# Kernel tuning notes

Measured on AMD Instinct MI355X. Metric: run time of the kernel, lower is better.

## Reference

```python
import math
import jax, jax.numpy as jnp
import numpy as np

B, N, D = 16, 2048, 64

def setup_inputs() -> dict:
    key = jax.random.key(0)
    kq, kk, kv, kl = jax.random.split(key, 4)
    q = jax.random.normal(kq, (B, N, D), dtype=jnp.float32)
    k = jax.random.normal(kk, (B, N, D), dtype=jnp.float32)
    v = jax.random.normal(kv, (B, N, D), dtype=jnp.float32)
    valid = jax.random.randint(kl, (B, N), 0, 2048, dtype=jnp.int64 if jax.config.jax_enable_x64 else jnp.int32)
    return {"q": q, "k": k, "v": v, "valid": valid}

def reference(q, k, v, valid):
    # scores[b,i,j] = <q[b,i], k[b,j]> / sqrt(d)
    d = k.shape[-1]
    scores = jnp.einsum('bid,bjd->bij', q, k) / jnp.sqrt(jnp.asarray(d, q.dtype))
    # mask[b,i,j] = (j+1) > valid[b,i]; masked positions replaced by 1e-6
    # (faithful to torch.masked_fill(scores, mask, 1e-06) -- NOT -inf)
    key_pos = jnp.arange(1, scores.shape[-1] + 1)  # [N]
    mask = key_pos[None, None, :] > valid[:, :, None]  # [B,N,N]
    mask_scores = jnp.where(mask, jnp.asarray(1e-06, scores.dtype), scores)
    weights = jax.nn.softmax(mask_scores, axis=-1)
    # dropout p=0.0 -> identity
    return jnp.einsum('bij,bjd->bid', weights, v)
```

## Files before the change

kernel.cpp:

```cpp
#include <hip/hip_runtime.h>
#include <hip/hip_bf16.h>
#include <stdint.h>

#define BB 16
#define NN 2048
#define DD 64
#define BM 64
#define BN 64
#define KSTR 72
#define PSTR 72

typedef __attribute__((ext_vector_type(8))) short short8;
typedef __attribute__((ext_vector_type(4))) float f32x4;

__device__ __forceinline__ unsigned short f2bf(float f) {
  union { float f; uint32_t u; } c; c.f = f;
  uint32_t u = c.u + 0x7fffu + ((c.u >> 16) & 1u);
  return (unsigned short)(u >> 16);
}
__device__ __forceinline__ uint32_t pkrn(float a, float b) {
  union { __hip_bfloat162 h; uint32_t u; } c;
  c.h = __float22bfloat162_rn(make_float2(a, b));
  return c.u;
}

__global__ __launch_bounds__(256) void prep_kernel(const float* __restrict__ k,
                                                   const float* __restrict__ v,
                                                   unsigned short* __restrict__ kbf,
                                                   unsigned short* __restrict__ vt) {
  __shared__ float t[64][65];
  int id = blockIdx.x, tid = threadIdx.x;
  if (id < 2048) {
    int i = id * 256 + tid;
    float4 f = ((const float4*)k)[i];
    ushort4 o;
    o.x = f2bf(f.x); o.y = f2bf(f.y); o.z = f2bf(f.z); o.w = f2bf(f.w);
    ((ushort4*)kbf)[i] = o;
  } else {
    int bid = id - 2048;
    int b = bid >> 5;
    int k0 = (bid & 31) * 64;
    const float4* src = (const float4*)(v + ((size_t)b * NN + k0) * DD);
#pragma unroll
    for (int i = 0; i < 4; i++) {
      int f4 = tid + i * 256;
      int row = f4 >> 4, c4 = f4 & 15;
      float4 f = src[f4];
      t[row][c4*4+0] = f.x; t[row][c4*4+1] = f.y; t[row][c4*4+2] = f.z; t[row][c4*4+3] = f.w;
    }
    __syncthreads();
    int d = tid >> 2, kg = tid & 3;
    unsigned short* dst = vt + ((size_t)b * DD + d) * NN + k0 + kg * 16;
#pragma unroll
    for (int u = 0; u < 4; u++) {
      ushort4 o;
      o.x = f2bf(t[kg*16+u*4+0][d]);
      o.y = f2bf(t[kg*16+u*4+1][d]);
      o.z = f2bf(t[kg*16+u*4+2][d]);
      o.w = f2bf(t[kg*16+u*4+3][d]);
      ((ushort4*)dst)[u] = o;
    }
  }
}

template <int NS>
__global__ __launch_bounds__(256, 4) void attn_kernel(
    const float* __restrict__ q, const unsigned short* __restrict__ kbf,
    const unsigned short* __restrict__ vtbf, const int* __restrict__ valid,
    float* __restrict__ out, unsigned short* __restrict__ po,
    float* __restrict__ pz)
{
  constexpr int JLEN = NN / NS;
  constexpr int ITERS = JLEN / BN;

  __shared__ __align__(16) unsigned short Klds[BN * KSTR];
  __shared__ __align__(16) unsigned short Vlds[DD * KSTR];
  __shared__ __align__(16) unsigned short Plds[4 * 16 * PSTR];
  __shared__ int vld[BM];

  int id = blockIdx.x;
  int b = (id & 7) + 8 * ((id >> 3) & 1);
  int rest = id >> 4;
  int sp = rest % NS;
  int qt = rest / NS;
  int i0 = qt * BM;
  int jbase = sp * JLEN;

  int tid = threadIdx.x;
  int w = tid >> 6;
  int lane = tid & 63;
  int m = lane & 15;
  int quad = lane >> 4;

  if (tid < BM) vld[tid] = valid[b * NN + i0 + tid];

  short8 qf[2];
  {
    const float* qp = q + ((size_t)b * NN + (i0 + w * 16 + m)) * DD;
#pragma unroll
    for (int s = 0; s < 2; s++) {
      float4 f0 = *(const float4*)(qp + s * 32 + quad * 8);
      float4 f1 = *(const float4*)(qp + s * 32 + quad * 8 + 4);
      union { short8 v; uint32_t x[4]; } tmp;
      tmp.x[0] = pkrn(f0.x * 0.125f, f0.y * 0.125f);
      tmp.x[1] = pkrn(f0.z * 0.125f, f0.w * 0.125f);
      tmp.x[2] = pkrn(f1.x * 0.125f, f1.y * 0.125f);
      tmp.x[3] = pkrn(f1.z * 0.125f, f1.w * 0.125f);
      qf[s] = tmp.v;
    }
  }

  __syncthreads();
  int vq = vld[w * 16 + m];

  f32x4 o[4] = {{0,0,0,0},{0,0,0,0},{0,0,0,0},{0,0,0,0}};
  float z = 0.0f;
  unsigned short* pbase = Plds + w * 16 * PSTR;

  int srow = tid >> 2, scol = (tid & 3) * 16;
  const unsigned short* gk = kbf + ((size_t)(b * NN + jbase + srow)) * DD + scol;
  const unsigned short* gv = vtbf + ((size_t)b * DD + srow) * NN + jbase + scol;

  uint4 ka = *(const uint4*)gk, kb2 = *(const uint4*)(gk + 8);
  uint4 va = *(const uint4*)gv, vb2 = *(const uint4*)(gv + 8);

  for (int it = 0; it < ITERS; ++it) {
    int j0 = jbase + it * BN;
    __syncthreads();
    *(uint4*)&Klds[srow * KSTR + scol]     = ka;
    *(uint4*)&Klds[srow * KSTR + scol + 8] = kb2;
    *(uint4*)&Vlds[srow * KSTR + scol]     = va;
    *(uint4*)&Vlds[srow * KSTR + scol + 8] = vb2;
    if (it + 1 < ITERS) {
      gk += BN * DD; gv += BN;
      ka = *(const uint4*)gk; kb2 = *(const uint4*)(gk + 8);
      va = *(const uint4*)gv; vb2 = *(const uint4*)(gv + 8);
    }
    __syncthreads();

    f32x4 s[4] = {{0,0,0,0},{0,0,0,0},{0,0,0,0},{0,0,0,0}};
#pragma unroll
    for (int c = 0; c < 4; c++) {
#pragma unroll
      for (int ss = 0; ss < 2; ss++) {
        short8 kf = *(const short8*)&Klds[(c * 16 + m) * KSTR + ss * 32 + quad * 8];
        s[c] = __builtin_amdgcn_mfma_f32_16x16x32_bf16(kf, qf[ss], s[c], 0, 0, 0);
      }
    }

#pragma unroll
    for (int c = 0; c < 4; c++) {
      float e[4];
#pragma unroll
      for (int rr = 0; rr < 4; rr++) {
        int j = j0 + c * 16 + quad * 4 + rr;
        float arg = (j < vq) ? s[c][rr] : 1.0e-6f;
        e[rr] = __expf(arg);
      }
      z += (e[0] + e[1]) + (e[2] + e[3]);
      *(uint2*)&pbase[m * PSTR + c * 16 + quad * 4] =
          make_uint2(pkrn(e[0], e[1]), pkrn(e[2], e[3]));
    }

    __builtin_amdgcn_s_waitcnt(0xc07f);

#pragma unroll
    for (int ss = 0; ss < 2; ss++) {
      short8 pf = *(const short8*)&pbase[m * PSTR + ss * 32 + quad * 8];
#pragma unroll
      for (int t = 0; t < 4; t++) {
        short8 vf = *(const short8*)&Vlds[(t * 16 + m) * KSTR + ss * 32 + quad * 8];
        o[t] = __builtin_amdgcn_mfma_f32_16x16x32_bf16(vf, pf, o[t], 0, 0, 0);
      }
    }
  }

  z += __shfl_xor(z, 16);
  z += __shfl_xor(z, 32);

  if (NS > 1) {
    int row = i0 + w * 16 + m;
    unsigned short* op = po + ((size_t)((sp * BB + b) * NN) + row) * DD;
#pragma unroll
    for (int t = 0; t < 4; t++)
      *(uint2*)&op[t * 16 + quad * 4] = make_uint2(pkrn(o[t][0], o[t][1]),
                                                   pkrn(o[t][2], o[t][3]));
    if (quad == 0) pz[(size_t)(sp * BB + b) * NN + row] = z;
  } else {
    float inv = 1.0f / z;
    int row = i0 + w * 16 + m;
    float* op = out + ((size_t)b * NN + row) * DD;
#pragma unroll
    for (int t = 0; t < 4; t++)
      *(float4*)&op[t * 16 + quad * 4] =
          make_float4(o[t][0]*inv, o[t][1]*inv, o[t][2]*inv, o[t][3]*inv);
  }
}

template <int NS>
__global__ __launch_bounds__(256) void combine_kernel(const unsigned short* __restrict__ po,
                                                      const float* __restrict__ pz,
                                                      float* __restrict__ out) {
  int gid = blockIdx.x * 256 + threadIdx.x;
  size_t base = (size_t)gid * 8;
  int rowz = gid >> 3;
  float r[8] = {0,0,0,0,0,0,0,0};
  float zs = 0.0f;
#pragma unroll
  for (int sp = 0; sp < NS; sp++) {
    uint4 a = *(const uint4*)(po + (size_t)sp * BB * NN * DD + base);
    zs += pz[(size_t)sp * BB * NN + rowz];
    uint32_t aw[4] = {a.x, a.y, a.z, a.w};
#pragma unroll
    for (int i = 0; i < 4; i++) {
      r[2*i]   += __uint_as_float(aw[i] << 16);
      r[2*i+1] += __uint_as_float(aw[i] & 0xffff0000u);
    }
  }
  float inv = 1.0f / zs;
  float4* op = (float4*)(out + base);
  op[0] = make_float4(r[0]*inv, r[1]*inv, r[2]*inv, r[3]*inv);
  op[1] = make_float4(r[4]*inv, r[5]*inv, r[6]*inv, r[7]*inv);
}

extern "C" void kernel_launch(void* const* d_in, const int* in_sizes, int n_in,
                              void* d_out, int out_size, void* d_ws, size_t ws_size,
                              hipStream_t stream) {
  const float* q = (const float*)d_in[0];
  const float* k = (const float*)d_in[1];
  const float* v = (const float*)d_in[2];
  const int* valid = (const int*)d_in[3];
  float* out = (float*)d_out;

  unsigned short* kbf  = (unsigned short*)d_ws;
  unsigned short* vtbf = kbf + (size_t)BB * NN * DD;
  unsigned short* po   = vtbf + (size_t)BB * NN * DD;
  float* pz4 = (float*)(po + (size_t)4 * BB * NN * DD);
  float* pz2 = (float*)(po + (size_t)2 * BB * NN * DD);

  size_t fixed = (size_t)2 * BB * NN * DD * 2;
  size_t need4 = fixed + (size_t)4 * BB * NN * DD * 2 + (size_t)4 * BB * NN * 4;
  size_t need2 = fixed + (size_t)2 * BB * NN * DD * 2 + (size_t)2 * BB * NN * 4;

  hipLaunchKernelGGL(prep_kernel, dim3(2560), dim3(256), 0, stream, k, v, kbf, vtbf);
  if (ws_size >= need4) {
    hipLaunchKernelGGL((attn_kernel<4>), dim3(16 * 32 * 4), dim3(256), 0, stream,
                       q, kbf, vtbf, valid, out, po, pz4);
    hipLaunchKernelGGL((combine_kernel<4>), dim3(1024), dim3(256), 0, stream, po, pz4, out);
  } else if (ws_size >= need2) {
    hipLaunchKernelGGL((attn_kernel<2>), dim3(16 * 32 * 2), dim3(256), 0, stream,
                       q, kbf, vtbf, valid, out, po, pz2);
    hipLaunchKernelGGL((combine_kernel<2>), dim3(1024), dim3(256), 0, stream, po, pz2, out);
  } else {
    hipLaunchKernelGGL((attn_kernel<1>), dim3(16 * 32), dim3(256), 0, stream,
                       q, kbf, vtbf, valid, out, po, pz2);
  }
}
```

Before: 115.8 us.

## Sort queries by valid length and replace fully masked key tiles with V suffix sums

A new prep stage counting-sorts each batch's query rows by their valid length and computes per-tile suffix sums of V. Each attention block processes sorted query tiles and iterates only over key tiles that some row in the tile can see. The skipped fully masked tiles are added analytically as exp(1e-6) times the suffix sum of V, and their count is added to the normaliser. This removes a large share of the MFMA and exp work, at the cost of an extra prep pass, scattered output writes through the permutation, and fp32 suffix-sum accumulation in place of bf16 products.

```diff
diff --git a/kernel.cpp b/kernel.cpp
--- a/kernel.cpp
+++ b/kernel.cpp
@@ -26,9 +26,16 @@
 
 __global__ __launch_bounds__(256) void prep_kernel(const float* __restrict__ k,
                                                    const float* __restrict__ v,
+                                                   const int* __restrict__ valid,
                                                    unsigned short* __restrict__ kbf,
-                                                   unsigned short* __restrict__ vt) {
+                                                   unsigned short* __restrict__ vt,
+                                                   int* __restrict__ perm,
+                                                   int* __restrict__ sval,
+                                                   float* __restrict__ suf) {
   __shared__ float t[64][65];
+  __shared__ int hist[2048];
+  __shared__ int part[256];
+  __shared__ float ts[32][16];
   int id = blockIdx.x, tid = threadIdx.x;
   if (id < 2048) {
     int i = id * 256 + tid;
@@ -36,7 +43,7 @@
     ushort4 o;
     o.x = f2bf(f.x); o.y = f2bf(f.y); o.z = f2bf(f.z); o.w = f2bf(f.w);
     ((ushort4*)kbf)[i] = o;
-  } else {
+  } else if (id < 2560) {
     int bid = id - 2048;
     int b = bid >> 5;
     int k0 = (bid & 31) * 64;
@@ -60,136 +67,210 @@
       o.w = f2bf(t[kg*16+u*4+3][d]);
       ((ushort4*)dst)[u] = o;
     }
+  } else if (id < 2576) {
+    int b = id - 2560;
+    for (int i = tid; i < 2048; i += 256) hist[i] = 0;
+    __syncthreads();
+    for (int i = tid; i < NN; i += 256) atomicAdd(&hist[valid[b * NN + i]], 1);
+    __syncthreads();
+    int base = tid * 8, loc[8], s = 0;
+#pragma unroll
+    for (int j = 0; j < 8; j++) { loc[j] = s; s += hist[base + j]; }
+    part[tid] = s;
+    __syncthreads();
+    if (tid == 0) {
+      int run = 0;
+      for (int t2 = 0; t2 < 256; t2++) { int tmp = part[t2]; part[t2] = run; run += tmp; }
+    }
+    __syncthreads();
+#pragma unroll
+    for (int j = 0; j < 8; j++) hist[base + j] = part[tid] + loc[j];
+    __syncthreads();
+    for (int i = tid; i < NN; i += 256) {
+      int vv = valid[b * NN + i];
+      int pos = atomicAdd(&hist[vv], 1);
+      perm[b * NN + pos] = i;
+      sval[b * NN + pos] = vv;
+    }
+  } else {
+    int sb = id - 2576;
+    int b = sb >> 2, dg = sb & 3;
+    for (int p = tid; p < 512; p += 256) {
+      int tt = p >> 4, d0 = p & 15;
+      const float* vp = v + ((size_t)b * NN + tt * 64) * DD + dg * 16 + d0;
+      float s = 0.0f;
+#pragma unroll 8
+      for (int r = 0; r < 64; r++) s += vp[(size_t)r * DD];
+      ts[tt][d0] = s;
+    }
+    __syncthreads();
+    if (tid < 16) {
+      int d = dg * 16 + tid;
+      float acc = 0.0f;
+      suf[((size_t)b * 33 + 32) * 64 + d] = 0.0f;
+      for (int tt = 31; tt >= 0; tt--) {
+        acc += ts[tt][tid];
+        suf[((size_t)b * 33 + tt) * 64 + d] = acc;
+      }
+    }
   }
 }
 
 template <int NS>
 __global__ __launch_bounds__(256, 4) void attn_kernel(
     const float* __restrict__ q, const unsigned short* __restrict__ kbf,
-    const unsigned short* __restrict__ vtbf, const int* __restrict__ valid,
+    const unsigned short* __restrict__ vtbf, const int* __restrict__ perm,
+    const int* __restrict__ sval, const float* __restrict__ suf,
     float* __restrict__ out, unsigned short* __restrict__ po,
     float* __restrict__ pz)
 {
   constexpr int JLEN = NN / NS;
-  constexpr int ITERS = JLEN / BN;
 
   __shared__ __align__(16) unsigned short Klds[BN * KSTR];
   __shared__ __align__(16) unsigned short Vlds[DD * KSTR];
   __shared__ __align__(16) unsigned short Plds[4 * 16 * PSTR];
   __shared__ int vld[BM];
+  __shared__ int pidx[BM];
 
   int id = blockIdx.x;
   int b = (id & 7) + 8 * ((id >> 3) & 1);
   int rest = id >> 4;
   int sp = rest % NS;
-  int qt = rest / NS;
+  int qt = 31 - (rest / NS);
   int i0 = qt * BM;
   int jbase = sp * JLEN;
+  int rangeEnd = jbase + JLEN;
 
   int tid = threadIdx.x;
-  int w = tid >> 6;
-  int lane = tid & 63;
-  int m = lane & 15;
-  int quad = lane >> 4;
-
-  if (tid < BM) vld[tid] = valid[b * NN + i0 + tid];
-
-  short8 qf[2];
-  {
-    const float* qp = q + ((size_t)b * NN + (i0 + w * 16 + m)) * DD;
-#pragma unroll
-    for (int s = 0; s < 2; s++) {
-      float4 f0 = *(const float4*)(qp + s * 32 + quad * 8);
-      float4 f1 = *(const float4*)(qp + s * 32 + quad * 8 + 4);
-      union { short8 v; uint32_t x[4]; } tmp;
-      tmp.x[0] = pkrn(f0.x * 0.125f, f0.y * 0.125f);
-      tmp.x[1] = pkrn(f0.z * 0.125f, f0.w * 0.125f);
-      tmp.x[2] = pkrn(f1.x * 0.125f, f1.y * 0.125f);
-      tmp.x[3] = pkrn(f1.z * 0.125f, f1.w * 0.125f);
-      qf[s] = tmp.v;
-    }
-  }
+  int w = tid >> 6, lane = tid & 63;
+  int m = lane & 15, quad = lane >> 4;
+
+  if (tid < BM) {
+    vld[tid]  = sval[b * NN + i0 + tid];
+    pidx[tid] = perm[b * NN + i0 + tid];
+  }
+  int maxv = sval[b * NN + i0 + 63];
+  int jcov = ((maxv + 63) >> 6) << 6;
+  int niter = (min(rangeEnd, jcov) - jbase) >> 6;
+  if (niter < 0) niter = 0;
+  int Tp = (jbase >> 6) + niter;
 
   __syncthreads();
-  int vq = vld[w * 16 + m];
 
   f32x4 o[4] = {{0,0,0,0},{0,0,0,0},{0,0,0,0},{0,0,0,0}};
   float z = 0.0f;
-  unsigned short* pbase = Plds + w * 16 * PSTR;
-
-  int srow = tid >> 2, scol = (tid & 3) * 16;
-  const unsigned short* gk = kbf + ((size_t)(b * NN + jbase + srow)) * DD + scol;
-  const unsigned short* gv = vtbf + ((size_t)b * DD + srow) * NN + jbase + scol;
-
-  uint4 ka = *(const uint4*)gk, kb2 = *(const uint4*)(gk + 8);
-  uint4 va = *(const uint4*)gv, vb2 = *(const uint4*)(gv + 8);
-
-  for (int it = 0; it < ITERS; ++it) {
-    int j0 = jbase + it * BN;
-    __syncthreads();
-    *(uint4*)&Klds[srow * KSTR + scol]     = ka;
-    *(uint4*)&Klds[srow * KSTR + scol + 8] = kb2;
-    *(uint4*)&Vlds[srow * KSTR + scol]     = va;
-    *(uint4*)&Vlds[srow * KSTR + scol + 8] = vb2;
-    if (it + 1 < ITERS) {
-      gk += BN * DD; gv += BN;
-      ka = *(const uint4*)gk; kb2 = *(const uint4*)(gk + 8);
-      va = *(const uint4*)gv; vb2 = *(const uint4*)(gv + 8);
-    }
-    __syncthreads();
-
-    f32x4 s[4] = {{0,0,0,0},{0,0,0,0},{0,0,0,0},{0,0,0,0}};
-#pragma unroll
-    for (int c = 0; c < 4; c++) {
+  const float CM = 1.0000010f;
+
+  if (niter > 0) {
+    int vq = vld[w * 16 + m];
+    int qrow = pidx[w * 16 + m];
+
+    short8 qf[2];
+    {
+      const float* qp = q + ((size_t)b * NN + qrow) * DD;
+#pragma unroll
+      for (int s = 0; s < 2; s++) {
+        float4 f0 = *(const float4*)(qp + s * 32 + quad * 8);
+        float4 f1 = *(const float4*)(qp + s * 32 + quad * 8 + 4);
+        union { short8 v; uint32_t x[4]; } tmp;
+        tmp.x[0] = pkrn(f0.x * 0.125f, f0.y * 0.125f);
+        tmp.x[1] = pkrn(f0.z * 0.125f, f0.w * 0.125f);
+        tmp.x[2] = pkrn(f1.x * 0.125f, f1.y * 0.125f);
+        tmp.x[3] = pkrn(f1.z * 0.125f, f1.w * 0.125f);
+        qf[s] = tmp.v;
+      }
+    }
+
+    unsigned short* pbase = Plds + w * 16 * PSTR;
+    int srow = tid >> 2, scol = (tid & 3) * 16;
+    const unsigned short* gk = kbf + ((size_t)(b * NN + jbase + srow)) * DD + scol;
+    const unsigned short* gv = vtbf + ((size_t)b * DD + srow) * NN + jbase + scol;
+
+    uint4 ka = *(const uint4*)gk, kb2 = *(const uint4*)(gk + 8);
+    uint4 va = *(const uint4*)gv, vb2 = *(const uint4*)(gv + 8);
+
+    for (int it = 0; it < niter; ++it) {
+      int j0 = jbase + it * BN;
+      __syncthreads();
+      *(uint4*)&Klds[srow * KSTR + scol]     = ka;
+      *(uint4*)&Klds[srow * KSTR + scol + 8] = kb2;
+      *(uint4*)&Vlds[srow * KSTR + scol]     = va;
+      *(uint4*)&Vlds[srow * KSTR + scol + 8] = vb2;
+      if (it + 1 < niter) {
+        gk += BN * DD; gv += BN;
+        ka = *(const uint4*)gk; kb2 = *(const uint4*)(gk + 8);
+        va = *(const uint4*)gv; vb2 = *(const uint4*)(gv + 8);
+      }
+      __syncthreads();
+
+      f32x4 s[4] = {{0,0,0,0},{0,0,0,0},{0,0,0,0},{0,0,0,0}};
+#pragma unroll
+      for (int c = 0; c < 4; c++) {
+#pragma unroll
+        for (int ss = 0; ss < 2; ss++) {
+          short8 kf = *(const short8*)&Klds[(c * 16 + m) * KSTR + ss * 32 + quad * 8];
+          s[c] = __builtin_amdgcn_mfma_f32_16x16x32_bf16(kf, qf[ss], s[c], 0, 0, 0);
+        }
+      }
+
+#pragma unroll
+      for (int c = 0; c < 4; c++) {
+        float e[4];
+#pragma unroll
+        for (int rr = 0; rr < 4; rr++) {
+          int j = j0 + c * 16 + quad * 4 + rr;
+          float arg = (j < vq) ? s[c][rr] : 1.0e-6f;
+          e[rr] = __expf(arg);
+        }
+        z += (e[0] + e[1]) + (e[2] + e[3]);
+        *(uint2*)&pbase[m * PSTR + c * 16 + quad * 4] =
+            make_uint2(pkrn(e[0], e[1]), pkrn(e[2], e[3]));
+      }
+
+      __builtin_amdgcn_s_waitcnt(0xc07f);
+
 #pragma unroll
       for (int ss = 0; ss < 2; ss++) {
-        short8 kf = *(const short8*)&Klds[(c * 16 + m) * KSTR + ss * 32 + quad * 8];
-        s[c] = __builtin_amdgcn_mfma_f32_16x16x32_bf16(kf, qf[ss], s[c], 0, 0, 0);
-      }
-    }
-
-#pragma unroll
-    for (int c = 0; c < 4; c++) {
-      float e[4];
-#pragma unroll
-      for (int rr = 0; rr < 4; rr++) {
-        int j = j0 + c * 16 + quad * 4 + rr;
-        float arg = (j < vq) ? s[c][rr] : 1.0e-6f;
-        e[rr] = __expf(arg);
-      }
-      z += (e[0] + e[1]) + (e[2] + e[3]);
-      *(uint2*)&pbase[m * PSTR + c * 16 + quad * 4] =
-          make_uint2(pkrn(e[0], e[1]), pkrn(e[2], e[3]));
-    }
-
-    __builtin_amdgcn_s_waitcnt(0xc07f);
-
-#pragma unroll
-    for (int ss = 0; ss < 2; ss++) {
-      short8 pf = *(const short8*)&pbase[m * PSTR + ss * 32 + quad * 8];
-#pragma unroll
-      for (int t = 0; t < 4; t++) {
-        short8 vf = *(const short8*)&Vlds[(t * 16 + m) * KSTR + ss * 32 + quad * 8];
-        o[t] = __builtin_amdgcn_mfma_f32_16x16x32_bf16(vf, pf, o[t], 0, 0, 0);
+        short8 pf = *(const short8*)&pbase[m * PSTR + ss * 32 + quad * 8];
+#pragma unroll
+        for (int t = 0; t < 4; t++) {
+          short8 vf = *(const short8*)&Vlds[(t * 16 + m) * KSTR + ss * 32 + quad * 8];
+          o[t] = __builtin_amdgcn_mfma_f32_16x16x32_bf16(vf, pf, o[t], 0, 0, 0);
+        }
       }
     }
   }
 
   z += __shfl_xor(z, 16);
   z += __shfl_xor(z, 32);
+  z += CM * (float)(rangeEnd - (Tp << 6));
+
+  {
+    const float* sh = suf + ((size_t)b * 33 + Tp) * 64;
+    const float* se = suf + ((size_t)b * 33 + (rangeEnd >> 6)) * 64;
+#pragma unroll
+    for (int t = 0; t < 4; t++) {
+      float4 a = *(const float4*)&sh[t * 16 + quad * 4];
+      float4 e4 = *(const float4*)&se[t * 16 + quad * 4];
+      o[t][0] += CM * (a.x - e4.x);
+      o[t][1] += CM * (a.y - e4.y);
+      o[t][2] += CM * (a.z - e4.z);
+      o[t][3] += CM * (a.w - e4.w);
+    }
+  }
 
   if (NS > 1) {
-    int row = i0 + w * 16 + m;
-    unsigned short* op = po + ((size_t)((sp * BB + b) * NN) + row) * DD;
+    int rrow = i0 + w * 16 + m;
+    unsigned short* op = po + ((size_t)((sp * BB + b) * NN) + rrow) * DD;
 #pragma unroll
     for (int t = 0; t < 4; t++)
       *(uint2*)&op[t * 16 + quad * 4] = make_uint2(pkrn(o[t][0], o[t][1]),
                                                    pkrn(o[t][2], o[t][3]));
-    if (quad == 0) pz[(size_t)(sp * BB + b) * NN + row] = z;
+    if (quad == 0) pz[(size_t)(sp * BB + b) * NN + rrow] = z;
   } else {
     float inv = 1.0f / z;
-    int row = i0 + w * 16 + m;
-    float* op = out + ((size_t)b * NN + row) * DD;
+    int qrow = pidx[w * 16 + m];
+    float* op = out + ((size_t)b * NN + qrow) * DD;
 #pragma unroll
     for (int t = 0; t < 4; t++)
       *(float4*)&op[t * 16 + quad * 4] =
@@ -200,16 +281,17 @@
 template <int NS>
 __global__ __launch_bounds__(256) void combine_kernel(const unsigned short* __restrict__ po,
                                                       const float* __restrict__ pz,
+                                                      const int* __restrict__ perm,
                                                       float* __restrict__ out) {
   int gid = blockIdx.x * 256 + threadIdx.x;
   size_t base = (size_t)gid * 8;
-  int rowz = gid >> 3;
+  int rowr = gid >> 3;
   float r[8] = {0,0,0,0,0,0,0,0};
   float zs = 0.0f;
 #pragma unroll
   for (int sp = 0; sp < NS; sp++) {
     uint4 a = *(const uint4*)(po + (size_t)sp * BB * NN * DD + base);
-    zs += pz[(size_t)sp * BB * NN + rowz];
+    zs += pz[(size_t)sp * BB * NN + rowr];
     uint32_t aw[4] = {a.x, a.y, a.z, a.w};
 #pragma unroll
     for (int i = 0; i < 4; i++) {
@@ -218,9 +300,11 @@
     }
   }
   float inv = 1.0f / zs;
-  float4* op = (float4*)(out + base);
-  op[0] = make_float4(r[0]*inv, r[1]*inv, r[2]*inv, r[3]*inv);
-  op[1] = make_float4(r[4]*inv, r[5]*inv, r[6]*inv, r[7]*inv);
+  int b = rowr >> 11;
+  int qrow = perm[rowr];
+  float* op = out + ((size_t)(b * NN + qrow)) * DD + (gid & 7) * 8;
+  *(float4*)&op[0] = make_float4(r[0]*inv, r[1]*inv, r[2]*inv, r[3]*inv);
+  *(float4*)&op[4] = make_float4(r[4]*inv, r[5]*inv, r[6]*inv, r[7]*inv);
 }
 
 extern "C" void kernel_launch(void* const* d_in, const int* in_sizes, int n_in,
@@ -235,24 +319,22 @@
   unsigned short* kbf  = (unsigned short*)d_ws;
   unsigned short* vtbf = kbf + (size_t)BB * NN * DD;
   unsigned short* po   = vtbf + (size_t)BB * NN * DD;
-  float* pz4 = (float*)(po + (size_t)4 * BB * NN * DD);
-  float* pz2 = (float*)(po + (size_t)2 * BB * NN * DD);
-
-  size_t fixed = (size_t)2 * BB * NN * DD * 2;
-  size_t need4 = fixed + (size_t)4 * BB * NN * DD * 2 + (size_t)4 * BB * NN * 4;
-  size_t need2 = fixed + (size_t)2 * BB * NN * DD * 2 + (size_t)2 * BB * NN * 4;
-
-  hipLaunchKernelGGL(prep_kernel, dim3(2560), dim3(256), 0, stream, k, v, kbf, vtbf);
+  float* pz   = (float*)(po + (size_t)4 * BB * NN * DD);
+  int*   perm = (int*)(pz + (size_t)4 * BB * NN);
+  int*   sv   = perm + (size_t)BB * NN;
+  float* suf  = (float*)(sv + (size_t)BB * NN);
+
+  size_t need4 = ((char*)(suf + (size_t)BB * 33 * DD)) - (char*)d_ws;
+
+  hipLaunchKernelGGL(prep_kernel, dim3(2640), dim3(256), 0, stream,
+                     k, v, valid, kbf, vtbf, perm, sv, suf);
   if (ws_size >= need4) {
     hipLaunchKernelGGL((attn_kernel<4>), dim3(16 * 32 * 4), dim3(256), 0, stream,
-                       q, kbf, vtbf, valid, out, po, pz4);
-    hipLaunchKernelGGL((combine_kernel<4>), dim3(1024), dim3(256), 0, stream, po, pz4, out);
-  } else if (ws_size >= need2) {
-    hipLaunchKernelGGL((attn_kernel<2>), dim3(16 * 32 * 2), dim3(256), 0, stream,
-                       q, kbf, vtbf, valid, out, po, pz2);
-    hipLaunchKernelGGL((combine_kernel<2>), dim3(1024), dim3(256), 0, stream, po, pz2, out);
+                       q, kbf, vtbf, perm, sv, suf, out, po, pz);
+    hipLaunchKernelGGL((combine_kernel<4>), dim3(1024), dim3(256), 0, stream,
+                       po, pz, perm, out);
   } else {
     hipLaunchKernelGGL((attn_kernel<1>), dim3(16 * 32), dim3(256), 0, stream,
-                       q, kbf, vtbf, valid, out, po, pz2);
-  }
-}
+                       q, kbf, vtbf, perm, sv, suf, out, po, pz);
+  }
+}
```

After: 116.4 us. About the same (+0.5%).
